# Kernel tuning notes

Measured on AMD Instinct MI355X. Metric: run time of the kernel, lower is better.

The kernel has to match this reference:

```python
import jax, jax.numpy as jnp
import numpy as np

INPUT_SIZE, HIDDEN, LAYERS, OUT_DIM = 256, 512, 2, 1
BATCH, SEQ = 64, 512


def _lstm_layer(x, W_ih, W_hh, b_ih, b_hh):
    # x: [B, T, D_in]; W_ih: [4H, D_in]; W_hh: [4H, H]; gate order i, f, g, o (PyTorch)
    B = x.shape[0]
    H = W_hh.shape[1]
    xg = jnp.einsum('btd,gd->btg', x, W_ih) + b_ih  # [B, T, 4H], input proj hoisted out of scan

    def step(carry, xg_t):
        h, c = carry
        g = xg_t + h @ W_hh.T + b_hh  # [B, 4H]
        i, f, gg, o = jnp.split(g, 4, axis=-1)
        c = jax.nn.sigmoid(f) * c + jax.nn.sigmoid(i) * jnp.tanh(gg)
        h = jax.nn.sigmoid(o) * jnp.tanh(c)
        return (h, c), h

    h0 = jnp.zeros((B, H), x.dtype)
    c0 = jnp.zeros((B, H), x.dtype)
    (hT, cT), hs = jax.lax.scan(step, (h0, c0), jnp.swapaxes(xg, 0, 1))
    return jnp.swapaxes(hs, 0, 1), hT, cT  # [B,T,H], [B,H], [B,H]


def setup_inputs() -> dict:
    key = jax.random.key(0)
    ks = jax.random.split(key, 12)
    s = 1.0 / np.sqrt(HIDDEN)
    u = lambda k, shape: jax.random.uniform(k, shape, jnp.float32, -s, s)
    return {
        'x': jax.random.normal(ks[0], (BATCH, SEQ, INPUT_SIZE), jnp.float32),
        'W_ih0': u(ks[1], (4 * HIDDEN, INPUT_SIZE)),
        'W_hh0': u(ks[2], (4 * HIDDEN, HIDDEN)),
        'b_ih0': u(ks[3], (4 * HIDDEN,)),
        'b_hh0': u(ks[4], (4 * HIDDEN,)),
        'W_ih1': u(ks[5], (4 * HIDDEN, HIDDEN)),
        'W_hh1': u(ks[6], (4 * HIDDEN, HIDDEN)),
        'b_ih1': u(ks[7], (4 * HIDDEN,)),
        'b_hh1': u(ks[8], (4 * HIDDEN,)),
        'fc_w': u(ks[9], (OUT_DIM, HIDDEN)),
        'fc_b': u(ks[10], (OUT_DIM,)),
    }


def reference(x, W_ih0, W_hh0, b_ih0, b_hh0, W_ih1, W_hh1, b_ih1, b_hh1, fc_w, fc_b):
    out0, h0T, c0T = _lstm_layer(x, W_ih0, W_hh0, b_ih0, b_hh0)
    out1, h1T, c1T = _lstm_layer(out0, W_ih1, W_hh1, b_ih1, b_hh1)
    out = out1[:, -1, :] @ fc_w.T + fc_b  # [B, OUT_DIM]
    hn = jnp.stack([h0T, h1T], axis=0)  # [layers, B, H]
    cn = jnp.stack([c0T, c1T], axis=0)
    return out, hn, cn
```

## Files before the change

### kernel.cpp

```cpp
#include <hip/hip_runtime.h>
#include <hip/hip_bf16.h>

#define B_   64
#define T_   512
#define DIN_ 256
#define H_   512

typedef __attribute__((ext_vector_type(2))) _Float16 h16x2;
typedef __attribute__((ext_vector_type(8))) _Float16 h16x8;
typedef __attribute__((ext_vector_type(2))) __fp16  fp16x2r;
typedef __attribute__((ext_vector_type(4))) float f32x4;
typedef unsigned short u16;
typedef unsigned long long u64;

__device__ __forceinline__ float sigmf(float xv) {
  return 1.0f / (1.0f + __expf(-xv));
}

__device__ __forceinline__ unsigned ld_flag_l2(const unsigned* p) {
  unsigned v;
  asm volatile("global_load_dword %0, %1, off sc0\n\ts_waitcnt vmcnt(0)"
               : "=v"(v) : "v"(p) : "memory");
  return v;
}
__device__ __forceinline__ void st_flag_l2(unsigned* p, unsigned v) {
  asm volatile("global_store_dword %0, %1, off sc0" :: "v"(p), "v"(v) : "memory");
}
#define LD16SC0(dst, p) \
  asm volatile("global_load_dwordx4 %0, %1, off sc0" : "=v"(dst) : "v"(p))
__device__ __forceinline__ void waitall16(h16x8* f) {
  asm volatile("s_waitcnt vmcnt(0)"
    : "+v"(f[0]), "+v"(f[1]), "+v"(f[2]),  "+v"(f[3]),
      "+v"(f[4]), "+v"(f[5]), "+v"(f[6]),  "+v"(f[7]),
      "+v"(f[8]), "+v"(f[9]), "+v"(f[10]), "+v"(f[11]),
      "+v"(f[12]),"+v"(f[13]),"+v"(f[14]), "+v"(f[15]) :: "memory");
}

__device__ __forceinline__ void waitL2(const unsigned* f, int lane) {
  int guard = 0;
  for (;;) {
    unsigned v = (lane < 32) ? ld_flag_l2(f + lane) : 1u;
    if (__all(v != 0u)) break;
    if (++guard > (1 << 20)) break;
  }
}
__device__ __forceinline__ void waitXC(const unsigned* f, int lane) {
  int guard = 0;
  for (;;) {
    unsigned v = (lane < 32)
      ? __hip_atomic_load((unsigned*)(f + lane), __ATOMIC_RELAXED, __HIP_MEMORY_SCOPE_AGENT)
      : 1u;
    if (__all(v != 0u)) break;
    if (++guard > (1 << 20)) break;
    __builtin_amdgcn_s_sleep(1);
  }
}
__device__ __forceinline__ h16x8 ldring(const u16* p) {
  union { h16x8 h; u64 q[2]; } u;
  u.q[0] = __hip_atomic_load((u64*)p,       __ATOMIC_RELAXED, __HIP_MEMORY_SCOPE_AGENT);
  u.q[1] = __hip_atomic_load((u64*)(p + 4), __ATOMIC_RELAXED, __HIP_MEMORY_SCOPE_AGENT);
  return u.h;
}

__device__ __forceinline__ h16x8 pk8(f32x4 a, f32x4 b) {
  union { h16x8 h; fp16x2r p[4]; } u;
  u.p[0] = __builtin_amdgcn_cvt_pkrtz(a.x, a.y);
  u.p[1] = __builtin_amdgcn_cvt_pkrtz(a.z, a.w);
  u.p[2] = __builtin_amdgcn_cvt_pkrtz(b.x, b.y);
  u.p[3] = __builtin_amdgcn_cvt_pkrtz(b.z, b.w);
  return u.h;
}

template <int LAYER>
__device__ __forceinline__ void lstm_body(
    const float* __restrict__ xin,
    const float* __restrict__ Wih, const float* __restrict__ Whh,
    const float* __restrict__ bih, const float* __restrict__ bhh,
    float* __restrict__ out,
    unsigned* __restrict__ iflags, unsigned* __restrict__ cf0,
    unsigned* __restrict__ cf1,
    u16* __restrict__ h0i, u16* __restrict__ h1i, u16* __restrict__ h0x,
    _Float16* wlds, int g, int j0, int slotW)
{
  constexpr int K    = LAYER ? 1024 : 768;
  constexpr int KP   = K + 8;
  constexpr int KIH  = LAYER ? 512 : 256;
  constexpr int NKB1 = KIH / 32;
  const int tid = threadIdx.x;

  {
    const int c = tid;
    if (c < (K >> 2)) {
      for (int rho = 0; rho < 64; ++rho) {
        const int gI = rho & 3, jI = (rho >> 2) & 3, nt = rho >> 4;
        const int gr = gI * H_ + j0 + nt * 4 + jI;
        f32x4 v;
        if (c < (KIH >> 2))
          v = *(const f32x4*)(Wih + (size_t)gr * KIH + (size_t)c * 4);
        else
          v = *(const f32x4*)(Whh + (size_t)gr * H_ + (size_t)(c - (KIH >> 2)) * 4);
        h16x2 q0, q1;
        q0[0] = (_Float16)v.x; q0[1] = (_Float16)v.y;
        q1[0] = (_Float16)v.z; q1[1] = (_Float16)v.w;
        *(h16x2*)(wlds + rho * KP + c * 4)     = q0;
        *(h16x2*)(wlds + rho * KP + c * 4 + 2) = q1;
      }
    }
  }

  const int lane = tid & 63;
  const int w    = tid >> 6;
  const int n    = lane & 15;
  const int quad = lane >> 4;
  const int gI   = n & 3;
  const int jI   = n >> 2;
  const int jglob = j0 + w * 4 + jI;
  const float bias = bih[gI * H_ + jglob] + bhh[gI * H_ + jglob];
  const int koffA = quad * 8;
  const _Float16* bbase = wlds + (w * 16 + n) * KP + koffA;

  __syncthreads();

  h16x8 bA[NKB1], bB[16];
#pragma unroll
  for (int kb = 0; kb < NKB1; ++kb) bA[kb] = *(const h16x8*)(bbase + kb * 32);
#pragma unroll
  for (int kb = 0; kb < 16; ++kb)   bB[kb] = *(const h16x8*)(bbase + KIH + kb * 32);

  unsigned* ifl  = iflags + (size_t)(LAYER * 4 + g) * T_ * 32;
  unsigned* cf0g = cf0 + (size_t)g * T_ * 32;
  unsigned* cf1g = cf1 + (size_t)g * T_ * 32;
  u16* myIr = LAYER ? (h1i + (size_t)g * 4 * 8192) : (h0i + (size_t)g * 8 * 8192);
  u16* h0xg = h0x + (size_t)g * 8 * 8192;

  f32x4 cst = {0.f, 0.f, 0.f, 0.f};

  for (int t = 0; t < T_; ++t) {
    f32x4 acc  = {0.f, 0.f, 0.f, 0.f};
    f32x4 acc2 = {0.f, 0.f, 0.f, 0.f};
    h16x8 ax[16];

    if (LAYER == 0) {
      const float* a0 = xin + (size_t)(g * 16 + n) * (T_ * DIN_) + (size_t)t * DIN_ + koffA;
#pragma unroll
      for (int kb = 0; kb < NKB1; ++kb) {
        h16x8 af = pk8(*(const f32x4*)(a0 + kb * 32), *(const f32x4*)(a0 + kb * 32 + 4));
        acc = __builtin_amdgcn_mfma_f32_16x16x32_f16(af, bA[kb], acc, 0, 0, 0);
      }
      if (t > 0) {
        waitL2(ifl + (size_t)(t - 1) * 32, lane);
        const u16* rb = myIr + (size_t)((t - 1) & 7) * 8192 + n * 512 + koffA;
        h16x8 fr[16];
#pragma unroll
        for (int kb = 0; kb < 16; ++kb) LD16SC0(fr[kb], rb + kb * 32);
        waitall16(fr);
#pragma unroll
        for (int kb = 0; kb < 16; ++kb)
          acc2 = __builtin_amdgcn_mfma_f32_16x16x32_f16(fr[kb], bB[kb], acc2, 0, 0, 0);
      }
      if (t >= 8) waitXC(cf1g + (size_t)(t - 8) * 32, lane);
    } else {
      waitXC(cf0g + (size_t)t * 32, lane);
      const u16* xb = h0xg + (size_t)(t & 7) * 8192 + n * 512 + koffA;
#pragma unroll
      for (int kb = 0; kb < 16; ++kb) ax[kb] = ldring(xb + kb * 32);
      if (t > 0) {
        waitL2(ifl + (size_t)(t - 1) * 32, lane);
        const u16* rb = myIr + (size_t)((t - 1) & 3) * 8192 + n * 512 + koffA;
        h16x8 fr[16];
#pragma unroll
        for (int kb = 0; kb < 16; ++kb) LD16SC0(fr[kb], rb + kb * 32);
        waitall16(fr);
#pragma unroll
        for (int kb = 0; kb < 16; ++kb)
          acc2 = __builtin_amdgcn_mfma_f32_16x16x32_f16(fr[kb], bB[kb], acc2, 0, 0, 0);
      }
#pragma unroll
      for (int kb = 0; kb < 16; ++kb)
        acc = __builtin_amdgcn_mfma_f32_16x16x32_f16(ax[kb], bA[kb], acc, 0, 0, 0);
    }

    u16* ringW = myIr + (size_t)(t & (LAYER ? 3 : 7)) * 8192;
    const bool lastT = (t == T_ - 1);
    const bool act = ((lane & 7) == 0);
    unsigned sv[4] = {0, 0, 0, 0};
#pragma unroll
    for (int r = 0; r < 4; ++r) {
      float pre = acc[r] + acc2[r] + bias;
      float vi = __shfl(pre, 0, 4);
      float vf = __shfl(pre, 1, 4);
      float vg = __shfl(pre, 2, 4);
      float vo = __shfl(pre, 3, 4);
      float tg  = 2.f * sigmf(2.f * vg) - 1.f;
      float cnv = sigmf(vf) * cst[r] + sigmf(vi) * tg;
      cst[r] = cnv;
      float hv = sigmf(vo) * (2.f * sigmf(2.f * cnv) - 1.f);
      float hv2 = __shfl(hv, lane + 4);
      const int m = quad * 4 + r;
      if (act) {
        _Float16 ha = (_Float16)hv, hb2 = (_Float16)hv2;
        union { struct { u16 a, b; } s; unsigned u; } pku;
        pku.s.a = *(const u16*)&ha; pku.s.b = *(const u16*)&hb2;
        *(unsigned*)&ringW[(size_t)m * 512 + jglob] = pku.u;
        sv[r] = pku.u;
      }
      if (lastT && (lane & 3) == 0) {
        const int gb = g * 16 + m;
        out[64 + LAYER * (B_ * H_) + gb * H_ + jglob] = hv;
        out[64 + 2 * (B_ * H_) + LAYER * (B_ * H_) + gb * H_ + jglob] = cnv;
      }
    }

    asm volatile("s_waitcnt vmcnt(0)" ::: "memory");
    __syncthreads();
    if (tid == 0) {
      st_flag_l2(ifl + (size_t)t * 32 + slotW, 1u);
      if (t > 0)
        __hip_atomic_store((LAYER ? cf1g : cf0g) + (size_t)(t - 1) * 32 + slotW, 1u,
                           __ATOMIC_RELAXED, __HIP_MEMORY_SCOPE_AGENT);
    }
    if (LAYER == 0 && act) {
      u16* xw = h0xg + (size_t)(t & 7) * 8192;
#pragma unroll
      for (int r = 0; r < 4; ++r)
        __hip_atomic_store((unsigned*)&xw[(size_t)(quad * 4 + r) * 512 + jglob], sv[r],
                           __ATOMIC_RELAXED, __HIP_MEMORY_SCOPE_AGENT);
    }
  }

  asm volatile("s_waitcnt vmcnt(0)" ::: "memory");
  __syncthreads();
  if (LAYER == 0 && tid == 0)
    __hip_atomic_store(cf0g + (size_t)(T_ - 1) * 32 + slotW, 1u,
                       __ATOMIC_RELAXED, __HIP_MEMORY_SCOPE_AGENT);
}

__global__ void __launch_bounds__(256, 1) lstm_kernel(
    const float* x,
    const float* Wih0, const float* Whh0, const float* bih0, const float* bhh0,
    const float* Wih1, const float* Whh1, const float* bih1, const float* bhh1,
    float* out, unsigned* claim, unsigned* iflags, unsigned* cf0, unsigned* cf1,
    u16* h0i, u16* h1i, u16* h0x)
{
  __shared__ unsigned role[2];
  extern __shared__ char smem[];
  _Float16* wlds = (_Float16*)smem;
  if (threadIdx.x == 0) {
    unsigned xcc = __builtin_amdgcn_s_getreg((31 << 11) | 20) & 7u;
    unsigned slot = __hip_atomic_fetch_add(&claim[xcc], 1u,
                                           __ATOMIC_RELAXED, __HIP_MEMORY_SCOPE_AGENT);
    role[0] = xcc; role[1] = slot & 31u;
  }
  __syncthreads();
  const int xcc = role[0], slotW = role[1];
  const int layer = xcc & 1, g = (xcc >> 1) & 3, j0 = slotW * 16;
  if (layer == 0)
    lstm_body<0>(x, Wih0, Whh0, bih0, bhh0, out, iflags, cf0, cf1,
                 h0i, h1i, h0x, wlds, g, j0, slotW);
  else
    lstm_body<1>(x, Wih1, Whh1, bih1, bhh1, out, iflags, cf0, cf1,
                 h0i, h1i, h0x, wlds, g, j0, slotW);
}

__global__ void init_kernel(unsigned* p, int nw) {
  int i = blockIdx.x * blockDim.x + threadIdx.x;
  for (; i < nw; i += gridDim.x * blockDim.x) p[i] = 0;
}

__global__ void fc_kernel(const float* __restrict__ hn1,
                          const float* __restrict__ fcw,
                          const float* __restrict__ fcb,
                          float* __restrict__ out) {
  const int tid = threadIdx.x;
  const int b = tid >> 2, q = tid & 3;
  const float* hr = hn1 + b * H_ + q * 128;
  const float* wr = fcw + q * 128;
  float s = 0.f;
  for (int i = 0; i < 128; ++i) s += hr[i] * wr[i];
  s += __shfl_xor(s, 1, 4);
  s += __shfl_xor(s, 2, 4);
  if (q == 0) out[b] = s + fcb[0];
}

extern "C" void kernel_launch(void* const* d_in, const int* in_sizes, int n_in,
                              void* d_out, int out_size, void* d_ws, size_t ws_size,
                              hipStream_t stream) {
  const float* x    = (const float*)d_in[0];
  const float* Wih0 = (const float*)d_in[1];
  const float* Whh0 = (const float*)d_in[2];
  const float* bih0 = (const float*)d_in[3];
  const float* bhh0 = (const float*)d_in[4];
  const float* Wih1 = (const float*)d_in[5];
  const float* Whh1 = (const float*)d_in[6];
  const float* bih1 = (const float*)d_in[7];
  const float* bhh1 = (const float*)d_in[8];
  const float* fcw  = (const float*)d_in[9];
  const float* fcb  = (const float*)d_in[10];
  float* out = (float*)d_out;

  unsigned* claim  = (unsigned*)d_ws;
  unsigned* iflags = (unsigned*)((char*)d_ws + 1024);
  unsigned* cf0    = (unsigned*)((char*)d_ws + 525312);
  unsigned* cf1    = (unsigned*)((char*)d_ws + 787456);
  u16* h0i = (u16*)((char*)d_ws + 1049600);
  u16* h1i = (u16*)((char*)d_ws + 1573888);
  u16* h0x = (u16*)((char*)d_ws + 1836032);

  init_kernel<<<256, 256, 0, stream>>>(claim, 262400);

  const int ldsBytes = 64 * (1024 + 8) * 2;
  (void)hipFuncSetAttribute((const void*)lstm_kernel,
                            hipFuncAttributeMaxDynamicSharedMemorySize, ldsBytes);
  lstm_kernel<<<256, 256, ldsBytes, stream>>>(x, Wih0, Whh0, bih0, bhh0,
                                              Wih1, Whh1, bih1, bhh1,
                                              out, claim, iflags, cf0, cf1,
                                              h0i, h1i, h0x);
  fc_kernel<<<1, 256, 0, stream>>>(out + 64 + B_ * H_, fcw, fcb, out);
}
```

Measured before the change: 3.933 ms.

## Stage recurrent h tiles cooperatively through LDS instead of per-wave global loads

Each of the four waves previously loaded the full 16x512 h tile from global/L2 for its MFMAs, giving four redundant reads per block per step. Now the block loads the tile once into padded LDS tiles, one 64-byte chunk per thread, then syncs, and the MFMAs read their operands from LDS. Layer 1's ring is deepened to 8 slots and the cross-layer flag for layer 1 is signalled on the current step instead of the previous one. The activation math is split into separate batched loops. This adds a __syncthreads per step and reuses the weight LDS region, which is safe only because weights were already copied into registers.

```diff
diff --git a/kernel.cpp b/kernel.cpp
--- a/kernel.cpp
+++ b/kernel.cpp
@@ -13,6 +13,8 @@
 typedef unsigned short u16;
 typedef unsigned long long u64;
 
+#define TSTRIDE 520
+
 __device__ __forceinline__ float sigmf(float xv) {
   return 1.0f / (1.0f + __expf(-xv));
 }
@@ -28,12 +30,9 @@
 }
 #define LD16SC0(dst, p) \
   asm volatile("global_load_dwordx4 %0, %1, off sc0" : "=v"(dst) : "v"(p))
-__device__ __forceinline__ void waitall16(h16x8* f) {
+__device__ __forceinline__ void waitall4(h16x8* f) {
   asm volatile("s_waitcnt vmcnt(0)"
-    : "+v"(f[0]), "+v"(f[1]), "+v"(f[2]),  "+v"(f[3]),
-      "+v"(f[4]), "+v"(f[5]), "+v"(f[6]),  "+v"(f[7]),
-      "+v"(f[8]), "+v"(f[9]), "+v"(f[10]), "+v"(f[11]),
-      "+v"(f[12]),"+v"(f[13]),"+v"(f[14]), "+v"(f[15]) :: "memory");
+    : "+v"(f[0]), "+v"(f[1]), "+v"(f[2]), "+v"(f[3]) :: "memory");
 }
 
 __device__ __forceinline__ void waitL2(const unsigned* f, int lane) {
@@ -71,6 +70,26 @@
   return u.h;
 }
 
+__device__ __forceinline__ void stage_intra(const u16* src, u16* dst, int tid) {
+  const int row = tid & 15, cb = tid >> 4;
+  const u16* s = src + row * 512 + cb * 32;
+  u16* d = dst + row * TSTRIDE + cb * 32;
+  h16x8 v[4];
+  LD16SC0(v[0], s);      LD16SC0(v[1], s + 8);
+  LD16SC0(v[2], s + 16); LD16SC0(v[3], s + 24);
+  waitall4(v);
+  *(h16x8*)(d)      = v[0]; *(h16x8*)(d + 8)  = v[1];
+  *(h16x8*)(d + 16) = v[2]; *(h16x8*)(d + 24) = v[3];
+}
+__device__ __forceinline__ void stage_cross(const u16* src, u16* dst, int tid) {
+  const int row = tid & 15, cb = tid >> 4;
+  const u16* s = src + row * 512 + cb * 32;
+  u16* d = dst + row * TSTRIDE + cb * 32;
+  h16x8 v0 = ldring(s), v1 = ldring(s + 8), v2 = ldring(s + 16), v3 = ldring(s + 24);
+  *(h16x8*)(d)      = v0; *(h16x8*)(d + 8)  = v1;
+  *(h16x8*)(d + 16) = v2; *(h16x8*)(d + 24) = v3;
+}
+
 template <int LAYER>
 __device__ __forceinline__ void lstm_body(
     const float* __restrict__ xin,
@@ -80,13 +99,14 @@
     unsigned* __restrict__ iflags, unsigned* __restrict__ cf0,
     unsigned* __restrict__ cf1,
     u16* __restrict__ h0i, u16* __restrict__ h1i, u16* __restrict__ h0x,
-    _Float16* wlds, int g, int j0, int slotW)
+    char* smem, int g, int j0, int slotW)
 {
   constexpr int K    = LAYER ? 1024 : 768;
   constexpr int KP   = K + 8;
   constexpr int KIH  = LAYER ? 512 : 256;
   constexpr int NKB1 = KIH / 32;
   const int tid = threadIdx.x;
+  _Float16* wlds = (_Float16*)smem;
 
   {
     const int c = tid;
@@ -127,18 +147,22 @@
 #pragma unroll
   for (int kb = 0; kb < 16; ++kb)   bB[kb] = *(const h16x8*)(bbase + KIH + kb * 32);
 
+  __syncthreads();
+
+  u16* tile0 = (u16*)smem;
+  u16* tile1 = (u16*)smem + 16 * TSTRIDE;
+
   unsigned* ifl  = iflags + (size_t)(LAYER * 4 + g) * T_ * 32;
   unsigned* cf0g = cf0 + (size_t)g * T_ * 32;
   unsigned* cf1g = cf1 + (size_t)g * T_ * 32;
-  u16* myIr = LAYER ? (h1i + (size_t)g * 4 * 8192) : (h0i + (size_t)g * 8 * 8192);
-  u16* h0xg = h0x + (size_t)g * 8 * 8192;
+  u16* myIr = (LAYER ? h1i : h0i) + (size_t)g * 65536;
+  u16* h0xg = h0x + (size_t)g * 65536;
 
   f32x4 cst = {0.f, 0.f, 0.f, 0.f};
 
   for (int t = 0; t < T_; ++t) {
     f32x4 acc  = {0.f, 0.f, 0.f, 0.f};
     f32x4 acc2 = {0.f, 0.f, 0.f, 0.f};
-    h16x8 ax[16];
 
     if (LAYER == 0) {
       const float* a0 = xin + (size_t)(g * 16 + n) * (T_ * DIN_) + (size_t)t * DIN_ + koffA;
@@ -149,65 +173,73 @@
       }
       if (t > 0) {
         waitL2(ifl + (size_t)(t - 1) * 32, lane);
-        const u16* rb = myIr + (size_t)((t - 1) & 7) * 8192 + n * 512 + koffA;
-        h16x8 fr[16];
-#pragma unroll
-        for (int kb = 0; kb < 16; ++kb) LD16SC0(fr[kb], rb + kb * 32);
-        waitall16(fr);
+        stage_intra(myIr + (size_t)((t - 1) & 7) * 8192, tile0, tid);
+        __syncthreads();
+        const _Float16* tp = (const _Float16*)tile0 + n * TSTRIDE + koffA;
 #pragma unroll
         for (int kb = 0; kb < 16; ++kb)
-          acc2 = __builtin_amdgcn_mfma_f32_16x16x32_f16(fr[kb], bB[kb], acc2, 0, 0, 0);
+          acc2 = __builtin_amdgcn_mfma_f32_16x16x32_f16(*(const h16x8*)(tp + kb * 32),
+                                                        bB[kb], acc2, 0, 0, 0);
       }
       if (t >= 8) waitXC(cf1g + (size_t)(t - 8) * 32, lane);
     } else {
       waitXC(cf0g + (size_t)t * 32, lane);
-      const u16* xb = h0xg + (size_t)(t & 7) * 8192 + n * 512 + koffA;
-#pragma unroll
-      for (int kb = 0; kb < 16; ++kb) ax[kb] = ldring(xb + kb * 32);
+      stage_cross(h0xg + (size_t)(t & 7) * 8192, tile1, tid);
       if (t > 0) {
         waitL2(ifl + (size_t)(t - 1) * 32, lane);
-        const u16* rb = myIr + (size_t)((t - 1) & 3) * 8192 + n * 512 + koffA;
-        h16x8 fr[16];
-#pragma unroll
-        for (int kb = 0; kb < 16; ++kb) LD16SC0(fr[kb], rb + kb * 32);
-        waitall16(fr);
+        stage_intra(myIr + (size_t)((t - 1) & 7) * 8192, tile0, tid);
+      }
+      __syncthreads();
+      if (t > 0) {
+        const _Float16* tp = (const _Float16*)tile0 + n * TSTRIDE + koffA;
 #pragma unroll
         for (int kb = 0; kb < 16; ++kb)
-          acc2 = __builtin_amdgcn_mfma_f32_16x16x32_f16(fr[kb], bB[kb], acc2, 0, 0, 0);
-      }
+          acc2 = __builtin_amdgcn_mfma_f32_16x16x32_f16(*(const h16x8*)(tp + kb * 32),
+                                                        bB[kb], acc2, 0, 0, 0);
+      }
+      const _Float16* xp = (const _Float16*)tile1 + n * TSTRIDE + koffA;
 #pragma unroll
       for (int kb = 0; kb < 16; ++kb)
-        acc = __builtin_amdgcn_mfma_f32_16x16x32_f16(ax[kb], bA[kb], acc, 0, 0, 0);
-    }
-
-    u16* ringW = myIr + (size_t)(t & (LAYER ? 3 : 7)) * 8192;
+        acc = __builtin_amdgcn_mfma_f32_16x16x32_f16(*(const h16x8*)(xp + kb * 32),
+                                                     bA[kb], acc, 0, 0, 0);
+    }
+
+    float pre[4], vi[4], vf[4], vg[4], vo[4], hv[4];
+#pragma unroll
+    for (int r = 0; r < 4; ++r) pre[r] = acc[r] + acc2[r] + bias;
+#pragma unroll
+    for (int r = 0; r < 4; ++r) {
+      vi[r] = __shfl(pre[r], 0, 4);
+      vf[r] = __shfl(pre[r], 1, 4);
+      vg[r] = __shfl(pre[r], 2, 4);
+      vo[r] = __shfl(pre[r], 3, 4);
+    }
+#pragma unroll
+    for (int r = 0; r < 4; ++r) {
+      float tg  = 2.f * sigmf(2.f * vg[r]) - 1.f;
+      float cnv = sigmf(vf[r]) * cst[r] + sigmf(vi[r]) * tg;
+      cst[r] = cnv;
+      hv[r] = sigmf(vo[r]) * (2.f * sigmf(2.f * cnv) - 1.f);
+    }
+
+    u16* ringW = myIr + (size_t)(t & 7) * 8192;
+    const bool act = ((lane & 7) == 0);
     const bool lastT = (t == T_ - 1);
-    const bool act = ((lane & 7) == 0);
-    unsigned sv[4] = {0, 0, 0, 0};
+    unsigned sv[4];
 #pragma unroll
     for (int r = 0; r < 4; ++r) {
-      float pre = acc[r] + acc2[r] + bias;
-      float vi = __shfl(pre, 0, 4);
-      float vf = __shfl(pre, 1, 4);
-      float vg = __shfl(pre, 2, 4);
-      float vo = __shfl(pre, 3, 4);
-      float tg  = 2.f * sigmf(2.f * vg) - 1.f;
-      float cnv = sigmf(vf) * cst[r] + sigmf(vi) * tg;
-      cst[r] = cnv;
-      float hv = sigmf(vo) * (2.f * sigmf(2.f * cnv) - 1.f);
-      float hv2 = __shfl(hv, lane + 4);
-      const int m = quad * 4 + r;
+      float hv2 = __shfl(hv[r], lane + 4);
       if (act) {
-        _Float16 ha = (_Float16)hv, hb2 = (_Float16)hv2;
+        _Float16 ha = (_Float16)hv[r], hb2 = (_Float16)hv2;
         union { struct { u16 a, b; } s; unsigned u; } pku;
         pku.s.a = *(const u16*)&ha; pku.s.b = *(const u16*)&hb2;
-        *(unsigned*)&ringW[(size_t)m * 512 + jglob] = pku.u;
         sv[r] = pku.u;
+        *(unsigned*)&ringW[(size_t)(quad * 4 + r) * 512 + jglob] = sv[r];
       }
       if (lastT && (lane & 3) == 0) {
-        const int gb = g * 16 + m;
-        out[64 + LAYER * (B_ * H_) + gb * H_ + jglob] = hv;
-        out[64 + 2 * (B_ * H_) + LAYER * (B_ * H_) + gb * H_ + jglob] = cnv;
+        const int gb = g * 16 + quad * 4 + r;
+        out[64 + LAYER * (B_ * H_) + gb * H_ + jglob] = hv[r];
+        out[64 + 2 * (B_ * H_) + LAYER * (B_ * H_) + gb * H_ + jglob] = cst[r];
       }
     }
 
@@ -215,9 +247,14 @@
     __syncthreads();
     if (tid == 0) {
       st_flag_l2(ifl + (size_t)t * 32 + slotW, 1u);
-      if (t > 0)
-        __hip_atomic_store((LAYER ? cf1g : cf0g) + (size_t)(t - 1) * 32 + slotW, 1u,
+      if (LAYER == 0) {
+        if (t > 0)
+          __hip_atomic_store(cf0g + (size_t)(t - 1) * 32 + slotW, 1u,
+                             __ATOMIC_RELAXED, __HIP_MEMORY_SCOPE_AGENT);
+      } else {
+        __hip_atomic_store(cf1g + (size_t)t * 32 + slotW, 1u,
                            __ATOMIC_RELAXED, __HIP_MEMORY_SCOPE_AGENT);
+      }
     }
     if (LAYER == 0 && act) {
       u16* xw = h0xg + (size_t)(t & 7) * 8192;
@@ -228,11 +265,13 @@
     }
   }
 
-  asm volatile("s_waitcnt vmcnt(0)" ::: "memory");
-  __syncthreads();
-  if (LAYER == 0 && tid == 0)
-    __hip_atomic_store(cf0g + (size_t)(T_ - 1) * 32 + slotW, 1u,
-                       __ATOMIC_RELAXED, __HIP_MEMORY_SCOPE_AGENT);
+  if (LAYER == 0) {
+    asm volatile("s_waitcnt vmcnt(0)" ::: "memory");
+    __syncthreads();
+    if (tid == 0)
+      __hip_atomic_store(cf0g + (size_t)(T_ - 1) * 32 + slotW, 1u,
+                         __ATOMIC_RELAXED, __HIP_MEMORY_SCOPE_AGENT);
+  }
 }
 
 __global__ void __launch_bounds__(256, 1) lstm_kernel(
@@ -244,7 +283,6 @@
 {
   __shared__ unsigned role[2];
   extern __shared__ char smem[];
-  _Float16* wlds = (_Float16*)smem;
   if (threadIdx.x == 0) {
     unsigned xcc = __builtin_amdgcn_s_getreg((31 << 11) | 20) & 7u;
     unsigned slot = __hip_atomic_fetch_add(&claim[xcc], 1u,
@@ -256,10 +294,10 @@
   const int layer = xcc & 1, g = (xcc >> 1) & 3, j0 = slotW * 16;
   if (layer == 0)
     lstm_body<0>(x, Wih0, Whh0, bih0, bhh0, out, iflags, cf0, cf1,
-                 h0i, h1i, h0x, wlds, g, j0, slotW);
+                 h0i, h1i, h0x, smem, g, j0, slotW);
   else
     lstm_body<1>(x, Wih1, Whh1, bih1, bhh1, out, iflags, cf0, cf1,
-                 h0i, h1i, h0x, wlds, g, j0, slotW);
+                 h0i, h1i, h0x, smem, g, j0, slotW);
 }
 
 __global__ void init_kernel(unsigned* p, int nw) {
@@ -304,7 +342,7 @@
   unsigned* cf1    = (unsigned*)((char*)d_ws + 787456);
   u16* h0i = (u16*)((char*)d_ws + 1049600);
   u16* h1i = (u16*)((char*)d_ws + 1573888);
-  u16* h0x = (u16*)((char*)d_ws + 1836032);
+  u16* h0x = (u16*)((char*)d_ws + 2098176);
 
   init_kernel<<<256, 256, 0, stream>>>(claim, 262400);
 
```

Result: slower. 4.091 ms (+4.0%).
